# Optimization experiments

Hardware: AMD Instinct MI355X
Metric: run time of the kernel (lower is better)

## Reference

```python
import jax, jax.numpy as jnp
import numpy as np

N_SAMPLES = 16384
L = 8000   # num pseudo labels
C = 8      # num cameras
D = 256    # feature dim
N = 512    # batch size
T = 0.05   # temperature
K = 50     # hard_neg_k
LW = 0.5   # inter-cam loss weight


def setup_inputs() -> dict:
    key = jax.random.key(0)
    k1, k2, k3, k4, k5 = jax.random.split(key, 5)
    feats = jax.random.normal(k1, (N, D), dtype=jnp.float32)
    indexes = jax.random.randint(k2, (N,), 0, N_SAMPLES)
    label_table = jax.random.randint(k3, (N_SAMPLES,), 0, L)
    cam_table = jax.random.randint(k4, (N_SAMPLES,), 0, C)
    centers = jax.random.normal(k5, (L * C, D), dtype=jnp.float32)
    centers = centers / jnp.linalg.norm(centers, axis=1, keepdims=True)
    return {"feats": feats, "indexes": indexes, "label_table": label_table,
            "cam_table": cam_table, "centers": centers}


def reference(feats, indexes, label_table, cam_table, centers):
    # F.normalize(feats, p=2, dim=1)
    feats = feats / jnp.linalg.norm(feats, axis=1, keepdims=True)
    labels = label_table[indexes]          # [n]
    cams = cam_table[indexes]              # [n]
    cen = jax.lax.stop_gradient(centers)   # centers are a non-grad buffer in torch

    all_sims = feats @ cen.T               # [n, P]  P = L*C, proxy(l,c) = l*C + c
    n, P = all_sims.shape
    sims_r = all_sims.reshape(n, L, C)     # [n, L, C]

    # ---- intra-camera loss: softmax over the L proxies sharing sample's camera ----
    idx_cam = jnp.broadcast_to(cams[:, None, None], (n, L, 1))
    sims_intra = jnp.take_along_axis(sims_r, idx_cam, axis=2)[..., 0]  # [n, L]
    logp_intra = jax.nn.log_softmax(sims_intra / T, axis=1)
    loss_intra_i = -jnp.take_along_axis(logp_intra, labels[:, None], axis=1)[:, 0]

    # ---- inter-camera loss: C positives (same label, all cams) + top-K hard negatives ----
    idx_lab = jnp.broadcast_to(labels[:, None, None], (n, 1, C))
    pos_sims = jnp.take_along_axis(sims_r, idx_lab, axis=1)[:, 0, :]   # [n, C]
    masked = jnp.where(jnp.arange(L)[None, :, None] == labels[:, None, None],
                       jnp.float32(-10000.0), sims_r).reshape(n, P)
    neg_sims, _ = jax.lax.top_k(masked, K)                             # [n, K]
    logits = jnp.concatenate([pos_sims, neg_sims], axis=1) / T         # [n, C+K]
    logp = jax.nn.log_softmax(logits, axis=1)
    loss_inter_i = -jnp.mean(logp[:, :C], axis=1)  # target = 1/C on the C positives

    # ---- per-camera mean, summed over cameras (matches the torch.unique loop) ----
    ones = jnp.ones((n,), feats.dtype)
    counts = jax.ops.segment_sum(ones, cams, num_segments=C)
    safe = jnp.maximum(counts, 1.0)
    s_intra = jax.ops.segment_sum(loss_intra_i, cams, num_segments=C)
    s_inter = jax.ops.segment_sum(loss_inter_i, cams, num_segments=C)
    loss_intra = jnp.sum(jnp.where(counts > 0, s_intra / safe, 0.0))
    loss_inter = LW * jnp.sum(jnp.where(counts > 0, s_inter / safe, 0.0))
    return jnp.stack([loss_intra, loss_inter])
```

## Files before the change

kernel.cpp:

```cpp
#include <hip/hip_runtime.h>
#include <stdint.h>

#define NS   512
#define DDIM 256
#define LL   8000
#define CC   8
#define PP   64000
#define KTOP 50
#define CAP  1024

typedef float f32x4 __attribute__((ext_vector_type(4)));
typedef short bf16x8 __attribute__((ext_vector_type(8)));
typedef short short8 __attribute__((ext_vector_type(8)));

__device__ __forceinline__ ushort f2bf(float x) {
    uint32_t b = __float_as_uint(x);
    b += 0x7fffu + ((b >> 16) & 1u);
    return (ushort)(b >> 16);
}
__device__ __forceinline__ float bf2f(ushort u) {
    return __uint_as_float(((uint32_t)u) << 16);
}

__global__ void k_norm_gather(const float* __restrict__ feats,
                              const int* __restrict__ indexes,
                              const int* __restrict__ ltab,
                              const int* __restrict__ ctab,
                              ushort* __restrict__ feats_b,
                              int* __restrict__ labels,
                              int* __restrict__ cams) {
    const int n = blockIdx.x;
    const int lane = threadIdx.x;
    f32x4 v = ((const f32x4*)(feats + (size_t)n * DDIM))[lane];
    float ss = v[0]*v[0] + v[1]*v[1] + v[2]*v[2] + v[3]*v[3];
#pragma unroll
    for (int off = 32; off > 0; off >>= 1) ss += __shfl_down(ss, off);
    float tot = __shfl(ss, 0);
    float sc = 1.0f / sqrtf(tot);
    ushort4 o;
    o.x = f2bf(v[0] * sc); o.y = f2bf(v[1] * sc);
    o.z = f2bf(v[2] * sc); o.w = f2bf(v[3] * sc);
    ((ushort4*)(feats_b + (size_t)n * DDIM))[lane] = o;
    if (lane == 0) {
        int idx = indexes[n];
        labels[n] = ltab[idx];
        cams[n] = ctab[idx];
    }
}

__global__ void k_conv_centers(const float* __restrict__ c, ushort* __restrict__ cb) {
    size_t i = (size_t)blockIdx.x * blockDim.x + threadIdx.x;
    size_t base = i * 8;
    f32x4 a = *(const f32x4*)(c + base);
    f32x4 b = *(const f32x4*)(c + base + 4);
    short8 r;
    r[0] = (short)f2bf(a[0]); r[1] = (short)f2bf(a[1]);
    r[2] = (short)f2bf(a[2]); r[3] = (short)f2bf(a[3]);
    r[4] = (short)f2bf(b[0]); r[5] = (short)f2bf(b[1]);
    r[6] = (short)f2bf(b[2]); r[7] = (short)f2bf(b[3]);
    *(short8*)(cb + base) = r;
}

template<bool F32S>
__global__ void k_gemm(const ushort* __restrict__ A, const ushort* __restrict__ B,
                       void* __restrict__ simsv) {
    const int lane = threadIdx.x & 63;
    const int w    = threadIdx.x >> 6;
    const int lr   = lane & 15;
    const int lk   = lane >> 4;
    const int bRow = blockIdx.y * 128;
    const int cBase = blockIdx.x * 128 + w * 32;

    f32x4 zero = {0.f, 0.f, 0.f, 0.f};
    f32x4 acc[8][2];
#pragma unroll
    for (int m = 0; m < 8; ++m) { acc[m][0] = zero; acc[m][1] = zero; }

#pragma unroll
    for (int kb = 0; kb < 8; ++kb) {
        const int kpos = kb * 32 + lk * 8;
        bf16x8 bfr[2];
#pragma unroll
        for (int nn = 0; nn < 2; ++nn)
            bfr[nn] = *(const bf16x8*)(B + (size_t)(cBase + nn * 16 + lr) * DDIM + kpos);
#pragma unroll
        for (int m = 0; m < 8; ++m) {
            bf16x8 afr = *(const bf16x8*)(A + (size_t)(bRow + m * 16 + lr) * DDIM + kpos);
            acc[m][0] = __builtin_amdgcn_mfma_f32_16x16x32_bf16(afr, bfr[0], acc[m][0], 0, 0, 0);
            acc[m][1] = __builtin_amdgcn_mfma_f32_16x16x32_bf16(afr, bfr[1], acc[m][1], 0, 0, 0);
        }
    }
#pragma unroll
    for (int m = 0; m < 8; ++m) {
#pragma unroll
        for (int nn = 0; nn < 2; ++nn) {
#pragma unroll
            for (int j = 0; j < 4; ++j) {
                int row = bRow + m * 16 + lk * 4 + j;
                int col = cBase + nn * 16 + lr;
                size_t idx = (size_t)row * PP + col;
                if constexpr (F32S) ((float*)simsv)[idx] = acc[m][nn][j];
                else                ((ushort*)simsv)[idx] = f2bf(acc[m][nn][j]);
            }
        }
    }
}

template<bool F32S>
__global__ __launch_bounds__(256) void k_persample(const void* __restrict__ simsv,
                                                   const int* __restrict__ labels,
                                                   const int* __restrict__ cams,
                                                   float* __restrict__ li,
                                                   float* __restrict__ le) {
    const int n = blockIdx.x;
    const int tid = threadIdx.x;
    const int label = labels[n];
    const int cam = cams[n];
    const float*  rf = (const float*)simsv + (size_t)n * PP;
    const ushort* rh = (const ushort*)simsv + (size_t)n * PP;

    __shared__ float cand[CAP];
    __shared__ float s_redA[256];
    __shared__ float s_redB[256];
    __shared__ int   s_cnt;
    __shared__ float s_tau, s_sig, s_sum, s_M;
    __shared__ float s_pos[CC];

    auto ld4 = [&](int g) -> f32x4 {
        if constexpr (F32S) {
            return ((const f32x4*)rf)[g];
        } else {
            ushort4 u = ((const ushort4*)rh)[g];
            f32x4 r; r[0] = bf2f(u.x); r[1] = bf2f(u.y); r[2] = bf2f(u.z); r[3] = bf2f(u.w);
            return r;
        }
    };
    auto ld1 = [&](int p) -> float {
        if constexpr (F32S) return rf[p];
        else return bf2f(rh[p]);
    };

    float lss = 0.0f, lcc = 0.0f;
#pragma unroll
    for (int i = 0; i < 8; ++i) {
        int g = tid + i * 256;
        int p0 = g * 4;
        if ((p0 >> 3) == label) continue;
        f32x4 v = ld4(g);
        lss += v[0]*v[0] + v[1]*v[1] + v[2]*v[2] + v[3]*v[3];
        lcc += 4.0f;
    }
    s_redA[tid] = lss; s_redB[tid] = lcc;
    __syncthreads();
    for (int off = 128; off > 0; off >>= 1) {
        if (tid < off) { s_redA[tid] += s_redA[tid + off]; s_redB[tid] += s_redB[tid + off]; }
        __syncthreads();
    }
    if (tid == 0) {
        float sig = sqrtf(s_redA[0] / fmaxf(s_redB[0], 1.0f));
        s_sig = sig;
        s_tau = 2.9f * sig;
    }

    const float K2 = 28.853900817779268f;
    float my_m = -1e30f, my_s = 0.0f;
    int pass = 0;
    int c;
    for (;;) {
        __syncthreads();
        if (tid == 0) s_cnt = 0;
        __syncthreads();
        float tau = s_tau;
        for (int g = tid; g < PP / 4; g += 256) {
            int p0 = g * 4;
            f32x4 v = ld4(g);
            if (pass == 0 && ((p0 & 4) == (cam & 4))) {
                float vi = (cam & 1) ? ((cam & 2) ? v[3] : v[1])
                                     : ((cam & 2) ? v[2] : v[0]);
                float y = vi * K2;
                if (y > my_m) { my_s = my_s * exp2f(my_m - y) + 1.0f; my_m = y; }
                else          { my_s += exp2f(y - my_m); }
            }
            if ((p0 >> 3) != label) {
#pragma unroll
                for (int j = 0; j < 4; ++j) {
                    if (v[j] > tau) {
                        int id = atomicAdd(&s_cnt, 1);
                        if (id < CAP) cand[id] = v[j];
                    }
                }
            }
        }
        __syncthreads();
        c = s_cnt;
        if ((c >= KTOP && c <= CAP) || pass >= 24) break;
        if (tid == 0) s_tau = (c < KTOP) ? (tau - 0.25f * s_sig) : (tau + 0.125f * s_sig);
        pass++;
    }
    if (c > CAP) c = CAP;

    s_redA[tid] = my_m; s_redB[tid] = my_s;
    __syncthreads();
    for (int off = 128; off > 0; off >>= 1) {
        if (tid < off) {
            float m1 = s_redA[tid],       s1 = s_redB[tid];
            float m2 = s_redA[tid + off], s2 = s_redB[tid + off];
            float M = fmaxf(m1, m2);
            s_redB[tid] = s1 * exp2f(m1 - M) + s2 * exp2f(m2 - M);
            s_redA[tid] = M;
        }
        __syncthreads();
    }
    if (tid == 0) {
        float lse_nat = 0.6931471805599453f * (s_redA[0] + log2f(s_redB[0]));
        float xl = ld1(label * CC + cam) * 20.0f;
        li[n] = lse_nat - xl;
    }
    if (tid < CC) s_pos[tid] = ld1(label * CC + tid);
    __syncthreads();

    float lm = -1e30f;
    for (int i = tid; i < c; i += 256) lm = fmaxf(lm, cand[i]);
    if (tid < CC) lm = fmaxf(lm, s_pos[tid]);
    s_redA[tid] = lm;
    __syncthreads();
    for (int off = 128; off > 0; off >>= 1) {
        if (tid < off) s_redA[tid] = fmaxf(s_redA[tid], s_redA[tid + off]);
        __syncthreads();
    }
    if (tid == 0) { s_M = s_redA[0]; s_sum = 0.0f; }
    __syncthreads();
    const float M = s_M;

    for (int i = tid; i < c; i += 256) {
        float v = cand[i];
        int r = 0;
        for (int j = 0; j < c; ++j) {
            float u = cand[j];
            r += (u > v) || (u == v && j < i);
        }
        if (r < KTOP) atomicAdd(&s_sum, exp2f((v - M) * K2));
    }
    if (tid < CC) atomicAdd(&s_sum, exp2f((s_pos[tid] - M) * K2));
    __syncthreads();
    if (tid == 0) {
        float possum = 0.0f;
#pragma unroll
        for (int j = 0; j < CC; ++j) possum += s_pos[j];
        float lse_nat = M * 20.0f + logf(s_sum);
        le[n] = lse_nat - possum * 20.0f / 8.0f;
    }
}

__global__ void k_finalize(const float* __restrict__ li, const float* __restrict__ le,
                           const int* __restrict__ cams, float* __restrict__ out) {
    __shared__ float si[CC], se[CC];
    __shared__ int sc[CC];
    int tid = threadIdx.x;
    if (tid < CC) { si[tid] = 0.f; se[tid] = 0.f; sc[tid] = 0; }
    __syncthreads();
    for (int i = tid; i < NS; i += 256) {
        int cm = cams[i];
        atomicAdd(&si[cm], li[i]);
        atomicAdd(&se[cm], le[i]);
        atomicAdd(&sc[cm], 1);
    }
    __syncthreads();
    if (tid == 0) {
        float a = 0.f, b = 0.f;
        for (int cm = 0; cm < CC; ++cm) {
            if (sc[cm] > 0) {
                a += si[cm] / (float)sc[cm];
                b += se[cm] / (float)sc[cm];
            }
        }
        out[0] = a;
        out[1] = 0.5f * b;
    }
}

extern "C" void kernel_launch(void* const* d_in, const int* in_sizes, int n_in,
                              void* d_out, int out_size, void* d_ws, size_t ws_size,
                              hipStream_t stream) {
    const float* feats   = (const float*)d_in[0];
    const int*   indexes = (const int*)d_in[1];
    const int*   ltab    = (const int*)d_in[2];
    const int*   ctab    = (const int*)d_in[3];
    const float* centers = (const float*)d_in[4];
    float* out = (float*)d_out;

    const size_t SZ_SIMS_F32 = (size_t)NS * PP * sizeof(float);
    const size_t SZ_SIMS_BF  = (size_t)NS * PP * sizeof(ushort);
    const size_t SZ_CB = (size_t)PP * DDIM * sizeof(ushort);
    const size_t SZ_FB = (size_t)NS * DDIM * sizeof(ushort);
    const size_t SMALL = 16 * 1024;

    const bool f32s = ws_size >= (SZ_SIMS_F32 + SZ_CB + SZ_FB + SMALL);

    char* p = (char*)d_ws;
    void* sims = (void*)p;       p += f32s ? SZ_SIMS_F32 : SZ_SIMS_BF;
    ushort* cb = (ushort*)p;     p += SZ_CB;
    ushort* fb = (ushort*)p;     p += SZ_FB;
    int* labels = (int*)p;       p += 2048;
    int* cams   = (int*)p;       p += 2048;
    float* li   = (float*)p;     p += 2048;
    float* le   = (float*)p;     p += 2048;

    hipLaunchKernelGGL(k_norm_gather, dim3(NS), dim3(64), 0, stream,
                       feats, indexes, ltab, ctab, fb, labels, cams);
    hipLaunchKernelGGL(k_conv_centers, dim3(8000), dim3(256), 0, stream, centers, cb);
    if (f32s) {
        hipLaunchKernelGGL((k_gemm<true>), dim3(500, 4), dim3(256), 0, stream, fb, cb, sims);
        hipLaunchKernelGGL((k_persample<true>), dim3(NS), dim3(256), 0, stream,
                           sims, labels, cams, li, le);
    } else {
        hipLaunchKernelGGL((k_gemm<false>), dim3(500, 4), dim3(256), 0, stream, fb, cb, sims);
        hipLaunchKernelGGL((k_persample<false>), dim3(NS), dim3(256), 0, stream,
                           sims, labels, cams, li, le);
    }
    hipLaunchKernelGGL(k_finalize, dim3(1), dim3(256), 0, stream, li, le, cams, out);
}
```

Before: 248.3 us.

## Fuse center bf16 conversion into GEMM and emit intra/positive sims from epilogue

Removes the separate centers-to-bf16 kernel by converting fp32 centers inside the GEMM, where each wave holds its B fragments in registers. The GEMM epilogue also writes the camera-matched intra-camera sims into a compact fp32 buffer and the per-label positive sims into a small buffer. The per-sample kernel then computes the intra-camera softmax and the sigma estimate from the compact buffer, and runs top-k thresholding over bf16 sims with 16-byte loads. The fp32 sims path is dropped, so the threshold search always runs on bf16 values, and the epilogue gains scattered conditional stores.

Measured after the change: 246.0 us. No clear change (-1.0%).

```diff
diff --git a/kernel.cpp b/kernel.cpp
--- a/kernel.cpp
+++ b/kernel.cpp
@@ -48,22 +48,11 @@
     }
 }
 
-__global__ void k_conv_centers(const float* __restrict__ c, ushort* __restrict__ cb) {
-    size_t i = (size_t)blockIdx.x * blockDim.x + threadIdx.x;
-    size_t base = i * 8;
-    f32x4 a = *(const f32x4*)(c + base);
-    f32x4 b = *(const f32x4*)(c + base + 4);
-    short8 r;
-    r[0] = (short)f2bf(a[0]); r[1] = (short)f2bf(a[1]);
-    r[2] = (short)f2bf(a[2]); r[3] = (short)f2bf(a[3]);
-    r[4] = (short)f2bf(b[0]); r[5] = (short)f2bf(b[1]);
-    r[6] = (short)f2bf(b[2]); r[7] = (short)f2bf(b[3]);
-    *(short8*)(cb + base) = r;
-}
-
-template<bool F32S>
-__global__ void k_gemm(const ushort* __restrict__ A, const ushort* __restrict__ B,
-                       void* __restrict__ simsv) {
+__global__ __launch_bounds__(256, 2)
+void k_gemm(const ushort* __restrict__ A, const float* __restrict__ B,
+            const int* __restrict__ labels, const int* __restrict__ cams,
+            ushort* __restrict__ sims, float* __restrict__ intrabuf,
+            float* __restrict__ posbuf) {
     const int lane = threadIdx.x & 63;
     const int w    = threadIdx.x >> 6;
     const int lr   = lane & 15;
@@ -71,6 +60,30 @@
     const int bRow = blockIdx.y * 128;
     const int cBase = blockIdx.x * 128 + w * 32;
 
+    __shared__ int s_lab[128], s_cam[128];
+    if (threadIdx.x < 128) {
+        s_lab[threadIdx.x] = labels[bRow + threadIdx.x];
+        s_cam[threadIdx.x] = cams[bRow + threadIdx.x];
+    }
+
+    bf16x8 bfr[2][8];
+#pragma unroll
+    for (int nn = 0; nn < 2; ++nn) {
+#pragma unroll
+        for (int kb = 0; kb < 8; ++kb) {
+            const float* src = B + (size_t)(cBase + nn * 16 + lr) * DDIM + kb * 32 + lk * 8;
+            f32x4 a = *(const f32x4*)src;
+            f32x4 b = *(const f32x4*)(src + 4);
+            bf16x8 r;
+            r[0] = (short)f2bf(a[0]); r[1] = (short)f2bf(a[1]);
+            r[2] = (short)f2bf(a[2]); r[3] = (short)f2bf(a[3]);
+            r[4] = (short)f2bf(b[0]); r[5] = (short)f2bf(b[1]);
+            r[6] = (short)f2bf(b[2]); r[7] = (short)f2bf(b[3]);
+            bfr[nn][kb] = r;
+        }
+    }
+    __syncthreads();
+
     f32x4 zero = {0.f, 0.f, 0.f, 0.f};
     f32x4 acc[8][2];
 #pragma unroll
@@ -79,45 +92,44 @@
 #pragma unroll
     for (int kb = 0; kb < 8; ++kb) {
         const int kpos = kb * 32 + lk * 8;
-        bf16x8 bfr[2];
-#pragma unroll
-        for (int nn = 0; nn < 2; ++nn)
-            bfr[nn] = *(const bf16x8*)(B + (size_t)(cBase + nn * 16 + lr) * DDIM + kpos);
 #pragma unroll
         for (int m = 0; m < 8; ++m) {
             bf16x8 afr = *(const bf16x8*)(A + (size_t)(bRow + m * 16 + lr) * DDIM + kpos);
-            acc[m][0] = __builtin_amdgcn_mfma_f32_16x16x32_bf16(afr, bfr[0], acc[m][0], 0, 0, 0);
-            acc[m][1] = __builtin_amdgcn_mfma_f32_16x16x32_bf16(afr, bfr[1], acc[m][1], 0, 0, 0);
-        }
-    }
+            acc[m][0] = __builtin_amdgcn_mfma_f32_16x16x32_bf16(afr, bfr[0][kb], acc[m][0], 0, 0, 0);
+            acc[m][1] = __builtin_amdgcn_mfma_f32_16x16x32_bf16(afr, bfr[1][kb], acc[m][1], 0, 0, 0);
+        }
+    }
+
 #pragma unroll
     for (int m = 0; m < 8; ++m) {
 #pragma unroll
         for (int nn = 0; nn < 2; ++nn) {
 #pragma unroll
             for (int j = 0; j < 4; ++j) {
-                int row = bRow + m * 16 + lk * 4 + j;
+                int rl  = m * 16 + lk * 4 + j;
+                int row = bRow + rl;
                 int col = cBase + nn * 16 + lr;
-                size_t idx = (size_t)row * PP + col;
-                if constexpr (F32S) ((float*)simsv)[idx] = acc[m][nn][j];
-                else                ((ushort*)simsv)[idx] = f2bf(acc[m][nn][j]);
+                float v = acc[m][nn][j];
+                sims[(size_t)row * PP + col] = f2bf(v);
+                int g = col >> 3, cc = col & 7;
+                if (g == s_lab[rl]) posbuf[row * CC + cc] = v;
+                if (cc == s_cam[rl]) intrabuf[(size_t)row * LL + g] = v;
             }
         }
     }
 }
 
-template<bool F32S>
-__global__ __launch_bounds__(256) void k_persample(const void* __restrict__ simsv,
-                                                   const int* __restrict__ labels,
-                                                   const int* __restrict__ cams,
-                                                   float* __restrict__ li,
-                                                   float* __restrict__ le) {
+__global__ __launch_bounds__(256)
+void k_persample(const ushort* __restrict__ sims, const float* __restrict__ intrabuf,
+                 const float* __restrict__ posbuf, const int* __restrict__ labels,
+                 const int* __restrict__ cams, float* __restrict__ li,
+                 float* __restrict__ le) {
     const int n = blockIdx.x;
     const int tid = threadIdx.x;
     const int label = labels[n];
     const int cam = cams[n];
-    const float*  rf = (const float*)simsv + (size_t)n * PP;
-    const ushort* rh = (const ushort*)simsv + (size_t)n * PP;
+    const ushort* row = sims + (size_t)n * PP;
+    const float* irow = intrabuf + (size_t)n * LL;
 
     __shared__ float cand[CAP];
     __shared__ float s_redA[256];
@@ -126,29 +138,20 @@
     __shared__ float s_tau, s_sig, s_sum, s_M;
     __shared__ float s_pos[CC];
 
-    auto ld4 = [&](int g) -> f32x4 {
-        if constexpr (F32S) {
-            return ((const f32x4*)rf)[g];
-        } else {
-            ushort4 u = ((const ushort4*)rh)[g];
-            f32x4 r; r[0] = bf2f(u.x); r[1] = bf2f(u.y); r[2] = bf2f(u.z); r[3] = bf2f(u.w);
-            return r;
-        }
-    };
-    auto ld1 = [&](int p) -> float {
-        if constexpr (F32S) return rf[p];
-        else return bf2f(rh[p]);
-    };
+    const float K2 = 28.853900817779268f;
 
     float lss = 0.0f, lcc = 0.0f;
-#pragma unroll
-    for (int i = 0; i < 8; ++i) {
-        int g = tid + i * 256;
-        int p0 = g * 4;
-        if ((p0 >> 3) == label) continue;
-        f32x4 v = ld4(g);
-        lss += v[0]*v[0] + v[1]*v[1] + v[2]*v[2] + v[3]*v[3];
-        lcc += 4.0f;
+    float my_m = -1e30f, my_s = 0.0f;
+    for (int g = tid; g < LL / 4; g += 256) {
+        f32x4 v = ((const f32x4*)irow)[g];
+#pragma unroll
+        for (int j = 0; j < 4; ++j) {
+            int l = g * 4 + j;
+            float y = v[j] * K2;
+            if (y > my_m) { my_s = my_s * exp2f(my_m - y) + 1.0f; my_m = y; }
+            else          { my_s += exp2f(y - my_m); }
+            if (l != label) { lss += v[j] * v[j]; lcc += 1.0f; }
+        }
     }
     s_redA[tid] = lss; s_redB[tid] = lcc;
     __syncthreads();
@@ -161,44 +164,7 @@
         s_sig = sig;
         s_tau = 2.9f * sig;
     }
-
-    const float K2 = 28.853900817779268f;
-    float my_m = -1e30f, my_s = 0.0f;
-    int pass = 0;
-    int c;
-    for (;;) {
-        __syncthreads();
-        if (tid == 0) s_cnt = 0;
-        __syncthreads();
-        float tau = s_tau;
-        for (int g = tid; g < PP / 4; g += 256) {
-            int p0 = g * 4;
-            f32x4 v = ld4(g);
-            if (pass == 0 && ((p0 & 4) == (cam & 4))) {
-                float vi = (cam & 1) ? ((cam & 2) ? v[3] : v[1])
-                                     : ((cam & 2) ? v[2] : v[0]);
-                float y = vi * K2;
-                if (y > my_m) { my_s = my_s * exp2f(my_m - y) + 1.0f; my_m = y; }
-                else          { my_s += exp2f(y - my_m); }
-            }
-            if ((p0 >> 3) != label) {
-#pragma unroll
-                for (int j = 0; j < 4; ++j) {
-                    if (v[j] > tau) {
-                        int id = atomicAdd(&s_cnt, 1);
-                        if (id < CAP) cand[id] = v[j];
-                    }
-                }
-            }
-        }
-        __syncthreads();
-        c = s_cnt;
-        if ((c >= KTOP && c <= CAP) || pass >= 24) break;
-        if (tid == 0) s_tau = (c < KTOP) ? (tau - 0.25f * s_sig) : (tau + 0.125f * s_sig);
-        pass++;
-    }
-    if (c > CAP) c = CAP;
-
+    __syncthreads();
     s_redA[tid] = my_m; s_redB[tid] = my_s;
     __syncthreads();
     for (int off = 128; off > 0; off >>= 1) {
@@ -213,11 +179,36 @@
     }
     if (tid == 0) {
         float lse_nat = 0.6931471805599453f * (s_redA[0] + log2f(s_redB[0]));
-        float xl = ld1(label * CC + cam) * 20.0f;
-        li[n] = lse_nat - xl;
-    }
-    if (tid < CC) s_pos[tid] = ld1(label * CC + tid);
-    __syncthreads();
+        li[n] = lse_nat - posbuf[n * CC + cam] * 20.0f;
+    }
+    if (tid < CC) s_pos[tid] = posbuf[n * CC + tid];
+
+    int pass = 0;
+    int c;
+    for (;;) {
+        __syncthreads();
+        if (tid == 0) s_cnt = 0;
+        __syncthreads();
+        float tau = s_tau;
+        for (int g = tid; g < LL; g += 256) {
+            if (g == label) continue;
+            short8 u = ((const short8*)row)[g];
+#pragma unroll
+            for (int j = 0; j < 8; ++j) {
+                float v = bf2f((ushort)u[j]);
+                if (v > tau) {
+                    int id = atomicAdd(&s_cnt, 1);
+                    if (id < CAP) cand[id] = v;
+                }
+            }
+        }
+        __syncthreads();
+        c = s_cnt;
+        if ((c >= KTOP && c <= CAP) || pass >= 24) break;
+        if (tid == 0) s_tau = (c < KTOP) ? (tau - 0.25f * s_sig) : (tau + 0.125f * s_sig);
+        pass++;
+    }
+    if (c > CAP) c = CAP;
 
     float lm = -1e30f;
     for (int i = tid; i < c; i += 256) lm = fmaxf(lm, cand[i]);
@@ -289,34 +280,26 @@
     const float* centers = (const float*)d_in[4];
     float* out = (float*)d_out;
 
-    const size_t SZ_SIMS_F32 = (size_t)NS * PP * sizeof(float);
-    const size_t SZ_SIMS_BF  = (size_t)NS * PP * sizeof(ushort);
-    const size_t SZ_CB = (size_t)PP * DDIM * sizeof(ushort);
-    const size_t SZ_FB = (size_t)NS * DDIM * sizeof(ushort);
-    const size_t SMALL = 16 * 1024;
-
-    const bool f32s = ws_size >= (SZ_SIMS_F32 + SZ_CB + SZ_FB + SMALL);
+    const size_t SZ_SIMS  = (size_t)NS * PP * sizeof(ushort);
+    const size_t SZ_INTRA = (size_t)NS * LL * sizeof(float);
+    const size_t SZ_POS   = (size_t)NS * CC * sizeof(float);
+    const size_t SZ_FB    = (size_t)NS * DDIM * sizeof(ushort);
 
     char* p = (char*)d_ws;
-    void* sims = (void*)p;       p += f32s ? SZ_SIMS_F32 : SZ_SIMS_BF;
-    ushort* cb = (ushort*)p;     p += SZ_CB;
-    ushort* fb = (ushort*)p;     p += SZ_FB;
-    int* labels = (int*)p;       p += 2048;
-    int* cams   = (int*)p;       p += 2048;
-    float* li   = (float*)p;     p += 2048;
-    float* le   = (float*)p;     p += 2048;
+    ushort* sims    = (ushort*)p;  p += SZ_SIMS;
+    float*  intrabf = (float*)p;   p += SZ_INTRA;
+    float*  posbuf  = (float*)p;   p += SZ_POS;
+    ushort* fb      = (ushort*)p;  p += SZ_FB;
+    int* labels = (int*)p;         p += 2048;
+    int* cams   = (int*)p;         p += 2048;
+    float* li   = (float*)p;       p += 2048;
+    float* le   = (float*)p;       p += 2048;
 
     hipLaunchKernelGGL(k_norm_gather, dim3(NS), dim3(64), 0, stream,
                        feats, indexes, ltab, ctab, fb, labels, cams);
-    hipLaunchKernelGGL(k_conv_centers, dim3(8000), dim3(256), 0, stream, centers, cb);
-    if (f32s) {
-        hipLaunchKernelGGL((k_gemm<true>), dim3(500, 4), dim3(256), 0, stream, fb, cb, sims);
-        hipLaunchKernelGGL((k_persample<true>), dim3(NS), dim3(256), 0, stream,
-                           sims, labels, cams, li, le);
-    } else {
-        hipLaunchKernelGGL((k_gemm<false>), dim3(500, 4), dim3(256), 0, stream, fb, cb, sims);
-        hipLaunchKernelGGL((k_persample<false>), dim3(NS), dim3(256), 0, stream,
-                           sims, labels, cams, li, le);
-    }
+    hipLaunchKernelGGL(k_gemm, dim3(500, 4), dim3(256), 0, stream,
+                       fb, centers, labels, cams, sims, intrabf, posbuf);
+    hipLaunchKernelGGL(k_persample, dim3(NS), dim3(256), 0, stream,
+                       sims, intrabf, posbuf, labels, cams, li, le);
     hipLaunchKernelGGL(k_finalize, dim3(1), dim3(256), 0, stream, li, le, cams, out);
 }
```
